# Performance work log

Hardware: AMD Instinct MI355X
Metric: run time of the kernel (lower is better)

## Reference

```python
import jax, jax.numpy as jnp
import numpy as np

N, E = 100000, 1600000
IN, EDGE_DIM, HID, OUT, HEADS = 128, 16, 32, 32, 2


def _glorot(key, shape, scale=0.1):
    return jax.random.normal(key, shape, dtype=jnp.float32) * scale


def setup_inputs() -> dict:
    key = jax.random.key(0)
    ks = jax.random.split(key, 20)
    HC1 = HEADS * HID
    return {
        "x": jax.random.normal(ks[0], (N, IN), dtype=jnp.float32),
        "edge_index": jax.random.randint(ks[1], (2, E), 0, N, dtype=jnp.int32),
        "edge_attr": jax.random.normal(ks[2], (E, EDGE_DIM), dtype=jnp.float32),
        # layer 1 (heads=HEADS, concat=True)
        "W1l": _glorot(ks[3], (IN, HC1)), "b1l": jnp.zeros((HC1,), jnp.float32),
        "W1r": _glorot(ks[4], (IN, HC1)), "b1r": jnp.zeros((HC1,), jnp.float32),
        "W1e": _glorot(ks[5], (EDGE_DIM, HC1)),
        "att1": _glorot(ks[6], (HEADS, HID)),
        "bias1": jnp.zeros((HC1,), jnp.float32),
        # layer 2 (heads=1, concat=False)
        "W2l": _glorot(ks[7], (HC1, HID)), "b2l": jnp.zeros((HID,), jnp.float32),
        "W2r": _glorot(ks[8], (HC1, HID)), "b2r": jnp.zeros((HID,), jnp.float32),
        "W2e": _glorot(ks[9], (EDGE_DIM, HID)),
        "att2": _glorot(ks[10], (1, HID)),
        "bias2": jnp.zeros((HID,), jnp.float32),
        # final linear
        "Wlin": _glorot(ks[11], (HID, OUT)), "blin": jnp.zeros((OUT,), jnp.float32),
    }


def gatv2_layer(x, src, dst, edge_attr, Wl, bl, Wr, br, We, att, bias, H, C, concat):
    n = x.shape[0]
    xl = (x @ Wl + bl).reshape(n, H, C)   # source transform (lin_l)
    xr = (x @ Wr + br).reshape(n, H, C)   # target transform (lin_r)
    ea = (edge_attr @ We).reshape(-1, H, C)
    m = xl[src] + xr[dst] + ea                       # [E, H, C]
    e = jnp.sum(jax.nn.leaky_relu(m, 0.2) * att, axis=-1)  # [E, H]
    # segment softmax over incoming edges of each destination node
    emax = jax.ops.segment_max(e, dst, num_segments=n)
    emax = jnp.where(jnp.isfinite(emax), emax, 0.0)
    ee = jnp.exp(e - emax[dst])
    denom = jax.ops.segment_sum(ee, dst, num_segments=n)
    alpha = ee / (denom[dst] + 1e-16)                # [E, H]
    out = jax.ops.segment_sum(xl[src] * alpha[..., None], dst, num_segments=n)  # [N, H, C]
    out = out.reshape(n, H * C) if concat else out.mean(axis=1)
    return out + bias


def reference(x, edge_index, edge_attr, W1l, b1l, W1r, b1r, W1e, att1, bias1,
              W2l, b2l, W2r, b2r, W2e, att2, bias2, Wlin, blin):
    src, dst = edge_index[0], edge_index[1]
    h = jax.nn.elu(gatv2_layer(x, src, dst, edge_attr, W1l, b1l, W1r, b1r, W1e,
                               att1, bias1, HEADS, HID, True))
    h = jax.nn.elu(gatv2_layer(h, src, dst, edge_attr, W2l, b2l, W2r, b2r, W2e,
                               att2, bias2, 1, HID, False))
    return h @ Wlin + blin
```

## Files before the change

kernel.cpp:

```cpp
#include <hip/hip_runtime.h>
#include <hip/hip_fp16.h>
#include <cstdint>
#include <cstddef>


typedef _Float16 half8 __attribute__((ext_vector_type(8)));
typedef float f32x4 __attribute__((ext_vector_type(4)));

__global__ void hist_kernel(const int* __restrict__ dst, int* __restrict__ deg, int E) {
    int e = blockIdx.x * blockDim.x + threadIdx.x;
    if (e < E) atomicAdd(&deg[dst[e]], 1);
}

__global__ void scan_part(const int* __restrict__ deg, int* __restrict__ bsum, int n) {
    int tid = threadIdx.x;
    int base = blockIdx.x * 1024 + tid * 4;
    int s = 0;
#pragma unroll
    for (int j = 0; j < 4; ++j) {
        int i = base + j;
        if (i < n) s += deg[i];
    }
#pragma unroll
    for (int off = 1; off < 64; off <<= 1) s += __shfl_xor(s, off, 64);
    __shared__ int ws[4];
    if ((tid & 63) == 0) ws[tid >> 6] = s;
    __syncthreads();
    if (tid == 0) bsum[blockIdx.x] = ws[0] + ws[1] + ws[2] + ws[3];
}

__global__ void scan_mid(int* __restrict__ bsum, int* __restrict__ rowstart, int nb, int n) {
    int tid = threadIdx.x;
    int v = (tid < nb) ? bsum[tid] : 0;
    int incl = v;
#pragma unroll
    for (int off = 1; off < 64; off <<= 1) {
        int t = __shfl_up(incl, off, 64);
        if ((tid & 63) >= off) incl += t;
    }
    __shared__ int w0;
    if (tid == 63) w0 = incl;
    __syncthreads();
    if (tid >= 64) incl += w0;
    if (tid < nb) bsum[tid] = incl - v;
    if (tid == nb - 1) rowstart[n] = incl;
}

__global__ void scan_fin(const int* __restrict__ deg, const int* __restrict__ bsum,
                         int* __restrict__ rowstart, int n) {
    int tid = threadIdx.x;
    int lane = tid & 63, wid = tid >> 6;
    int base = blockIdx.x * 1024 + tid * 4;
    int v[4];
    int s = 0;
#pragma unroll
    for (int j = 0; j < 4; ++j) {
        int i = base + j;
        v[j] = (i < n) ? deg[i] : 0;
        s += v[j];
    }
    int incl = s;
#pragma unroll
    for (int off = 1; off < 64; off <<= 1) {
        int t = __shfl_up(incl, off, 64);
        if (lane >= off) incl += t;
    }
    __shared__ int ws[4];
    if (lane == 63) ws[wid] = incl;
    __syncthreads();
    int wofs = 0;
    for (int w2 = 0; w2 < wid; ++w2) wofs += ws[w2];
    int acc = bsum[blockIdx.x] + wofs + (incl - s);
#pragma unroll
    for (int j = 0; j < 4; ++j) {
        int i = base + j;
        if (i < n) rowstart[i] = acc;
        acc += v[j];
    }
}

__global__ void scatter_kernel(const int* __restrict__ src, const int* __restrict__ dst,
                               const int* __restrict__ rowstart, int* __restrict__ cursor,
                               int2* __restrict__ es, int E) {
    int e = blockIdx.x * blockDim.x + threadIdx.x;
    if (e < E) {
        int d = dst[e];
        int p = atomicAdd(&cursor[d], 1);
        es[rowstart[d] + p] = make_int2(e, src[e]);
    }
}

__global__ void f2h_kernel(const float* __restrict__ in, __half* __restrict__ out, long n8) {
    long i = (long)blockIdx.x * blockDim.x + threadIdx.x;
    if (i < n8) {
        const float4* s = (const float4*)&in[i * 8];
        float4 a = s[0], b = s[1];
        __half2* d = (__half2*)&out[i * 8];
        d[0] = __float22half2_rn(make_float2(a.x, a.y));
        d[1] = __float22half2_rn(make_float2(a.z, a.w));
        d[2] = __float22half2_rn(make_float2(b.x, b.y));
        d[3] = __float22half2_rn(make_float2(b.z, b.w));
    }
}

template <int K, int Mh>
__global__ void wprep_kernel(const float* __restrict__ Wl, const float* __restrict__ Wr,
                             __half* __restrict__ Wfrag) {
    constexpr int KS = K / 32;
    constexpr int BN = 2 * Mh;
    int i = blockIdx.x * blockDim.x + threadIdx.x;
    if (i >= K * BN) return;
    int j = i & 7;
    int lane = (i >> 3) & 63;
    int rest = i >> 9;
    int ks = rest % KS;
    int nt = rest / KS;
    int k = ks * 32 + ((lane >> 4) & 3) * 8 + j;
    int col = nt * 16 + (lane & 15);
    float v = (col < Mh) ? Wl[k * Mh + col] : Wr[k * Mh + (col - Mh)];
    Wfrag[i] = __float2half(v);
}

template <int K, int Mh, int BM>
__global__ __launch_bounds__(256) void gemm_mfma(
    const float* __restrict__ x, const __half* __restrict__ Wfrag,
    const float* __restrict__ bl, const float* __restrict__ br,
    __half* __restrict__ yl, __half* __restrict__ yr, int n) {
    constexpr int BN = 2 * Mh;
    constexpr int KS = K / 32;
    constexpr int NT = BN / 16;
    constexpr int RW = BM / 64;
    constexpr int LDP = K + 8;
    __shared__ __half xs[BM * LDP];
    int tid = threadIdx.x;
    int lane = tid & 63;
    int wave = tid >> 6;
    int node0 = blockIdx.x * BM;
    constexpr int ITER = (BM * K) / (256 * 4);
#pragma unroll
    for (int it = 0; it < ITER; ++it) {
        int base = (it * 256 + tid) * 4;
        int row = base / K, kk = base % K;
        float4 v = make_float4(0.f, 0.f, 0.f, 0.f);
        if (node0 + row < n) v = *(const float4*)&x[(size_t)(node0 + row) * K + kk];
        __half2* d = (__half2*)&xs[row * LDP + kk];
        d[0] = __float22half2_rn(make_float2(v.x, v.y));
        d[1] = __float22half2_rn(make_float2(v.z, v.w));
    }
    __syncthreads();
    f32x4 acc[RW][NT];
#pragma unroll
    for (int r = 0; r < RW; ++r)
#pragma unroll
        for (int t = 0; t < NT; ++t) {
            f32x4 z = {0.f, 0.f, 0.f, 0.f};
            acc[r][t] = z;
        }
    int r0 = lane & 15, kof = (lane >> 4) * 8;
#pragma unroll
    for (int ks = 0; ks < KS; ++ks) {
        half8 a[RW];
#pragma unroll
        for (int r = 0; r < RW; ++r) {
            int row = (wave * RW + r) * 16 + r0;
            a[r] = *reinterpret_cast<const half8*>(&xs[row * LDP + ks * 32 + kof]);
        }
#pragma unroll
        for (int t = 0; t < NT; ++t) {
            half8 b = *reinterpret_cast<const half8*>(&Wfrag[(((size_t)t * KS + ks) * 64 + lane) * 8]);
#pragma unroll
            for (int r = 0; r < RW; ++r)
                acc[r][t] = __builtin_amdgcn_mfma_f32_16x16x32_f16(a[r], b, acc[r][t], 0, 0, 0);
        }
    }
#pragma unroll
    for (int r = 0; r < RW; ++r) {
#pragma unroll
        for (int t = 0; t < NT; ++t) {
            int col = t * 16 + (lane & 15);
            float bv = (col < Mh) ? bl[col] : br[col - Mh];
#pragma unroll
            for (int q = 0; q < 4; ++q) {
                int node = node0 + (wave * RW + r) * 16 + (lane >> 4) * 4 + q;
                if (node < n) {
                    float v = acc[r][t][q] + bv;
                    if (col < Mh) yl[(size_t)node * Mh + col] = __float2half(v);
                    else          yr[(size_t)node * Mh + (col - Mh)] = __float2half(v);
                }
            }
        }
    }
}

template <int K, int M, int NPB>
__global__ void linear_kernel(const float* __restrict__ x, const float* __restrict__ W,
                              const float* __restrict__ b, float* __restrict__ y, int n) {
    __shared__ float sx[NPB * K];
    int tid = threadIdx.x;
    int node0 = blockIdx.x * NPB;
    for (int i = tid; i < NPB * K; i += NPB * M) {
        int nn = node0 + i / K;
        sx[i] = (nn < n) ? x[(size_t)nn * K + (i % K)] : 0.f;
    }
    __syncthreads();
    int ln = tid / M, m = tid % M;
    int node = node0 + ln;
    if (node >= n) return;
    float acc = b[m];
#pragma unroll
    for (int k = 0; k < K; ++k) acc = fmaf(sx[ln * K + k], W[k * M + m], acc);
    y[(size_t)node * M + m] = acc;
}

template <int H, int C>
__global__ __launch_bounds__(256) void fused_edge_agg(
    const int* __restrict__ rowstart, const int2* __restrict__ es,
    const __half* __restrict__ eah,
    const float* __restrict__ We,
    const float* __restrict__ att,
    const __half* __restrict__ xl, const __half* __restrict__ xr,
    const float* __restrict__ bias, float* __restrict__ out, int n) {
    constexpr int HC = H * C;
    constexpr int LPN = HC / 2;
    constexpr int NPW = 64 / LPN;
    int gt = blockIdx.x * blockDim.x + threadIdx.x;
    int wave = gt >> 6;
    int lane = threadIdx.x & 63;
    int sub = lane / LPN;
    int j = lane % LPN;
    int ch0 = 2 * j;
    int node = wave * NPW + sub;
    if (node >= n) return;
    __half2 wh[16];
#pragma unroll
    for (int k = 0; k < 16; ++k) wh[k] = __float22half2_rn(*(const float2*)&We[k * HC + ch0]);
    float2 a2 = *(const float2*)&att[ch0];
    float2 xr2 = __half22float2(*(const __half2*)&xr[(size_t)node * HC + ch0]);
    int beg = rowstart[node], end = rowstart[node + 1];
    float denom = 0.f, acc0 = 0.f, acc1 = 0.f;

    auto gemv = [&](const float4& r0, const float4& r1, const __half2& xlh,
                    float& m0, float& m1, float2& xlf) {
        const __half2* h0 = (const __half2*)&r0;
        const __half2* h1 = (const __half2*)&r1;
        __half2 p0 = __hmul2(__low2half2(h0[0]), wh[0]);
        __half2 p1 = __hmul2(__high2half2(h0[0]), wh[1]);
        p0 = __hfma2(__low2half2(h0[1]), wh[2], p0);
        p1 = __hfma2(__high2half2(h0[1]), wh[3], p1);
        p0 = __hfma2(__low2half2(h0[2]), wh[4], p0);
        p1 = __hfma2(__high2half2(h0[2]), wh[5], p1);
        p0 = __hfma2(__low2half2(h0[3]), wh[6], p0);
        p1 = __hfma2(__high2half2(h0[3]), wh[7], p1);
        p0 = __hfma2(__low2half2(h1[0]), wh[8], p0);
        p1 = __hfma2(__high2half2(h1[0]), wh[9], p1);
        p0 = __hfma2(__low2half2(h1[1]), wh[10], p0);
        p1 = __hfma2(__high2half2(h1[1]), wh[11], p1);
        p0 = __hfma2(__low2half2(h1[2]), wh[12], p0);
        p1 = __hfma2(__high2half2(h1[2]), wh[13], p1);
        p0 = __hfma2(__low2half2(h1[3]), wh[14], p0);
        p1 = __hfma2(__high2half2(h1[3]), wh[15], p1);
        float2 mf = __half22float2(__hadd2(p0, p1));
        xlf = __half22float2(xlh);
        m0 = xlf.x + xr2.x + mf.x;
        m1 = xlf.y + xr2.y + mf.y;
    };
    auto logit = [&](float m0, float m1) -> float {
        m0 = (m0 > 0.f) ? m0 : 0.2f * m0;
        m1 = (m1 > 0.f) ? m1 : 0.2f * m1;
        float v = m0 * a2.x + m1 * a2.y;
#pragma unroll
        for (int msk = 1; msk < 16; msk <<= 1) v += __shfl_xor(v, msk, 64);
        return v;
    };

    int pp = beg;
    for (; pp + 4 <= end; pp += 4) {
        int2 er[4];
        float4 r0[4], r1[4];
        __half2 xh[4];
#pragma unroll
        for (int u = 0; u < 4; ++u) er[u] = es[pp + u];
#pragma unroll
        for (int u = 0; u < 4; ++u) {
            const float4* q = (const float4*)&eah[(size_t)er[u].x * 16];
            r0[u] = q[0];
            r1[u] = q[1];
            xh[u] = *(const __half2*)&xl[(size_t)er[u].y * HC + ch0];
        }
#pragma unroll
        for (int u = 0; u < 4; ++u) {
            float m0, m1;
            float2 xlf;
            gemv(r0[u], r1[u], xh[u], m0, m1, xlf);
            float w = __expf(logit(m0, m1));
            denom += w;
            acc0 = fmaf(xlf.x, w, acc0);
            acc1 = fmaf(xlf.y, w, acc1);
        }
    }
    for (; pp < end; ++pp) {
        int2 e2 = es[pp];
        const float4* q = (const float4*)&eah[(size_t)e2.x * 16];
        float4 r0 = q[0], r1 = q[1];
        __half2 xlh = *(const __half2*)&xl[(size_t)e2.y * HC + ch0];
        float m0, m1;
        float2 xlf;
        gemv(r0, r1, xlh, m0, m1, xlf);
        float w = __expf(logit(m0, m1));
        denom += w;
        acc0 = fmaf(xlf.x, w, acc0);
        acc1 = fmaf(xlf.y, w, acc1);
    }
    float2 b2 = *(const float2*)&bias[ch0];
    float inv = 1.f / (denom + 1e-16f);
    float o0 = acc0 * inv + b2.x;
    float o1 = acc1 * inv + b2.y;
    o0 = (o0 > 0.f) ? o0 : __expf(o0) - 1.f;
    o1 = (o1 > 0.f) ? o1 : __expf(o1) - 1.f;
    *(float2*)&out[(size_t)node * HC + ch0] = make_float2(o0, o1);
}

extern "C" void kernel_launch(void* const* d_in, const int* in_sizes, int n_in,
                              void* d_out, int out_size, void* d_ws, size_t ws_size,
                              hipStream_t stream) {
    const float* x     = (const float*)d_in[0];
    const int*   eidx  = (const int*)d_in[1];
    const float* eattr = (const float*)d_in[2];
    const float* W1l   = (const float*)d_in[3];
    const float* b1l   = (const float*)d_in[4];
    const float* W1r   = (const float*)d_in[5];
    const float* b1r   = (const float*)d_in[6];
    const float* W1e   = (const float*)d_in[7];
    const float* att1  = (const float*)d_in[8];
    const float* bias1 = (const float*)d_in[9];
    const float* W2l   = (const float*)d_in[10];
    const float* b2l   = (const float*)d_in[11];
    const float* W2r   = (const float*)d_in[12];
    const float* b2r   = (const float*)d_in[13];
    const float* W2e   = (const float*)d_in[14];
    const float* att2  = (const float*)d_in[15];
    const float* bias2 = (const float*)d_in[16];
    const float* Wlin  = (const float*)d_in[17];
    const float* blin  = (const float*)d_in[18];

    const int N = in_sizes[0] / 128;
    const int E = in_sizes[1] / 2;
    const int* src = eidx;
    const int* dst = eidx + E;

    char* p = (char*)d_ws;
    auto take = [&](size_t bytes) {
        char* r = p;
        p += (bytes + 255) & ~(size_t)255;
        return r;
    };
    int*    deg      = (int*)take((size_t)N * sizeof(int));
    int*    cursor   = (int*)take((size_t)N * sizeof(int));
    int*    rowstart = (int*)take((size_t)(N + 1) * sizeof(int));
    int*    bsum     = (int*)take(256 * sizeof(int));
    int2*   es       = (int2*)take((size_t)E * sizeof(int2));
    __half* A        = (__half*)take((size_t)N * 64 * sizeof(__half));
    __half* B        = (__half*)take((size_t)N * 64 * sizeof(__half));
    float*  Cbuf     = (float*)take((size_t)N * 64 * sizeof(float));
    __half* eah      = (__half*)take((size_t)E * 16 * sizeof(__half));
    __half* Wf1      = (__half*)take((size_t)128 * 128 * sizeof(__half));
    __half* Wf2      = (__half*)take((size_t)64 * 64 * sizeof(__half));

    (void)hipMemsetAsync(deg, 0, (size_t)N * sizeof(int), stream);
    (void)hipMemsetAsync(cursor, 0, (size_t)N * sizeof(int), stream);
    hist_kernel<<<(E + 255) / 256, 256, 0, stream>>>(dst, deg, E);
    {
        int nb = (N + 1023) / 1024;
        scan_part<<<nb, 256, 0, stream>>>(deg, bsum, N);
        scan_mid<<<1, 128, 0, stream>>>(bsum, rowstart, nb, N);
        scan_fin<<<nb, 256, 0, stream>>>(deg, bsum, rowstart, N);
    }
    scatter_kernel<<<(E + 255) / 256, 256, 0, stream>>>(src, dst, rowstart, cursor, es, E);
    {
        long n8 = (long)E * 16 / 8;
        f2h_kernel<<<(int)((n8 + 255) / 256), 256, 0, stream>>>(eattr, eah, n8);
    }
    wprep_kernel<128, 64><<<(128 * 128 + 255) / 256, 256, 0, stream>>>(W1l, W1r, Wf1);
    wprep_kernel<64, 32><<<(64 * 64 + 255) / 256, 256, 0, stream>>>(W2l, W2r, Wf2);

    gemm_mfma<128, 64, 64><<<(N + 63) / 64, 256, 0, stream>>>(x, Wf1, b1l, b1r, A, B, N);
    fused_edge_agg<2, 32><<<(int)(((size_t)((N + 1) / 2) * 64 + 255) / 256), 256, 0, stream>>>(
        rowstart, es, eah, W1e, att1, A, B, bias1, Cbuf, N);

    gemm_mfma<64, 32, 128><<<(N + 127) / 128, 256, 0, stream>>>(Cbuf, Wf2, b2l, b2r, A, B, N);
    fused_edge_agg<1, 32><<<(int)(((size_t)((N + 3) / 4) * 64 + 255) / 256), 256, 0, stream>>>(
        rowstart, es, eah, W2e, att2, A, B, bias2, Cbuf, N);

    linear_kernel<32, 32, 8><<<(N + 7) / 8, 256, 0, stream>>>(Cbuf, Wlin, blin, (float*)d_out, N);
}
```

Baseline: 444.1 us.

## Store edge attributes in dst-sorted order during scatter and drop f2h kernel

The scatter kernel now converts each edge's attributes to fp16 and writes them at the edge's CSR position, alongside a plain sorted source-index array. The separate f2h conversion kernel and the edge-id indirection are gone. The edge aggregation kernels therefore read attributes contiguously instead of gathering them by edge id, and the main loop unroll drops from 4 to 2. The scatter kernel's random-position writes grow from 8 to 36 bytes per edge, and the shallower unroll may expose more load latency.

Measured after the change: 457.9 us. 3.1% more time.

```diff
diff --git a/kernel.cpp b/kernel.cpp
--- a/kernel.cpp
+++ b/kernel.cpp
@@ -80,26 +80,30 @@
 }
 
 __global__ void scatter_kernel(const int* __restrict__ src, const int* __restrict__ dst,
+                               const float* __restrict__ eattr,
                                const int* __restrict__ rowstart, int* __restrict__ cursor,
-                               int2* __restrict__ es, int E) {
+                               int* __restrict__ src_sorted, __half* __restrict__ eah_sorted,
+                               int E) {
     int e = blockIdx.x * blockDim.x + threadIdx.x;
     if (e < E) {
         int d = dst[e];
         int p = atomicAdd(&cursor[d], 1);
-        es[rowstart[d] + p] = make_int2(e, src[e]);
-    }
-}
-
-__global__ void f2h_kernel(const float* __restrict__ in, __half* __restrict__ out, long n8) {
-    long i = (long)blockIdx.x * blockDim.x + threadIdx.x;
-    if (i < n8) {
-        const float4* s = (const float4*)&in[i * 8];
-        float4 a = s[0], b = s[1];
-        __half2* d = (__half2*)&out[i * 8];
-        d[0] = __float22half2_rn(make_float2(a.x, a.y));
-        d[1] = __float22half2_rn(make_float2(a.z, a.w));
-        d[2] = __float22half2_rn(make_float2(b.x, b.y));
-        d[3] = __float22half2_rn(make_float2(b.z, b.w));
+        int pos = rowstart[d] + p;
+        src_sorted[pos] = src[e];
+        const float4* s4 = (const float4*)&eattr[(size_t)e * 16];
+        float4 a = s4[0], b = s4[1], c = s4[2], f = s4[3];
+        __half2 h[8];
+        h[0] = __float22half2_rn(make_float2(a.x, a.y));
+        h[1] = __float22half2_rn(make_float2(a.z, a.w));
+        h[2] = __float22half2_rn(make_float2(b.x, b.y));
+        h[3] = __float22half2_rn(make_float2(b.z, b.w));
+        h[4] = __float22half2_rn(make_float2(c.x, c.y));
+        h[5] = __float22half2_rn(make_float2(c.z, c.w));
+        h[6] = __float22half2_rn(make_float2(f.x, f.y));
+        h[7] = __float22half2_rn(make_float2(f.z, f.w));
+        int4* o = (int4*)&eah_sorted[(size_t)pos * 16];
+        o[0] = *(int4*)&h[0];
+        o[1] = *(int4*)&h[4];
     }
 }
 
@@ -214,8 +218,8 @@
 
 template <int H, int C>
 __global__ __launch_bounds__(256) void fused_edge_agg(
-    const int* __restrict__ rowstart, const int2* __restrict__ es,
-    const __half* __restrict__ eah,
+    const int* __restrict__ rowstart, const int* __restrict__ src_sorted,
+    const __half* __restrict__ eah_sorted,
     const float* __restrict__ We,
     const float* __restrict__ att,
     const __half* __restrict__ xl, const __half* __restrict__ xr,
@@ -274,42 +278,39 @@
     };
 
     int pp = beg;
-    for (; pp + 4 <= end; pp += 4) {
-        int2 er[4];
-        float4 r0[4], r1[4];
-        __half2 xh[4];
-#pragma unroll
-        for (int u = 0; u < 4; ++u) er[u] = es[pp + u];
-#pragma unroll
-        for (int u = 0; u < 4; ++u) {
-            const float4* q = (const float4*)&eah[(size_t)er[u].x * 16];
-            r0[u] = q[0];
-            r1[u] = q[1];
-            xh[u] = *(const __half2*)&xl[(size_t)er[u].y * HC + ch0];
-        }
-#pragma unroll
-        for (int u = 0; u < 4; ++u) {
-            float m0, m1;
-            float2 xlf;
-            gemv(r0[u], r1[u], xh[u], m0, m1, xlf);
-            float w = __expf(logit(m0, m1));
-            denom += w;
-            acc0 = fmaf(xlf.x, w, acc0);
-            acc1 = fmaf(xlf.y, w, acc1);
-        }
-    }
-    for (; pp < end; ++pp) {
-        int2 e2 = es[pp];
-        const float4* q = (const float4*)&eah[(size_t)e2.x * 16];
-        float4 r0 = q[0], r1 = q[1];
-        __half2 xlh = *(const __half2*)&xl[(size_t)e2.y * HC + ch0];
-        float m0, m1;
-        float2 xlf;
-        gemv(r0, r1, xlh, m0, m1, xlf);
-        float w = __expf(logit(m0, m1));
-        denom += w;
-        acc0 = fmaf(xlf.x, w, acc0);
-        acc1 = fmaf(xlf.y, w, acc1);
+    for (; pp + 2 <= end; pp += 2) {
+        int s0 = src_sorted[pp];
+        int s1 = src_sorted[pp + 1];
+        const float4* qa = (const float4*)&eah_sorted[(size_t)pp * 16];
+        const float4* qb = (const float4*)&eah_sorted[((size_t)pp + 1) * 16];
+        float4 r0a = qa[0], r1a = qa[1];
+        float4 r0b = qb[0], r1b = qb[1];
+        __half2 xh0 = *(const __half2*)&xl[(size_t)s0 * HC + ch0];
+        __half2 xh1 = *(const __half2*)&xl[(size_t)s1 * HC + ch0];
+        float m0a, m1a, m0b, m1b;
+        float2 xla, xlb;
+        gemv(r0a, r1a, xh0, m0a, m1a, xla);
+        gemv(r0b, r1b, xh1, m0b, m1b, xlb);
+        float wa = __expf(logit(m0a, m1a));
+        float wb = __expf(logit(m0b, m1b));
+        denom += wa + wb;
+        acc0 = fmaf(xla.x, wa, acc0);
+        acc1 = fmaf(xla.y, wa, acc1);
+        acc0 = fmaf(xlb.x, wb, acc0);
+        acc1 = fmaf(xlb.y, wb, acc1);
+    }
+    if (pp < end) {
+        int s0 = src_sorted[pp];
+        const float4* qa = (const float4*)&eah_sorted[(size_t)pp * 16];
+        float4 r0a = qa[0], r1a = qa[1];
+        __half2 xh0 = *(const __half2*)&xl[(size_t)s0 * HC + ch0];
+        float m0a, m1a;
+        float2 xla;
+        gemv(r0a, r1a, xh0, m0a, m1a, xla);
+        float wa = __expf(logit(m0a, m1a));
+        denom += wa;
+        acc0 = fmaf(xla.x, wa, acc0);
+        acc1 = fmaf(xla.y, wa, acc1);
     }
     float2 b2 = *(const float2*)&bias[ch0];
     float inv = 1.f / (denom + 1e-16f);
@@ -354,17 +355,17 @@
         p += (bytes + 255) & ~(size_t)255;
         return r;
     };
-    int*    deg      = (int*)take((size_t)N * sizeof(int));
-    int*    cursor   = (int*)take((size_t)N * sizeof(int));
-    int*    rowstart = (int*)take((size_t)(N + 1) * sizeof(int));
-    int*    bsum     = (int*)take(256 * sizeof(int));
-    int2*   es       = (int2*)take((size_t)E * sizeof(int2));
-    __half* A        = (__half*)take((size_t)N * 64 * sizeof(__half));
-    __half* B        = (__half*)take((size_t)N * 64 * sizeof(__half));
-    float*  Cbuf     = (float*)take((size_t)N * 64 * sizeof(float));
-    __half* eah      = (__half*)take((size_t)E * 16 * sizeof(__half));
-    __half* Wf1      = (__half*)take((size_t)128 * 128 * sizeof(__half));
-    __half* Wf2      = (__half*)take((size_t)64 * 64 * sizeof(__half));
+    int*    deg        = (int*)take((size_t)N * sizeof(int));
+    int*    cursor     = (int*)take((size_t)N * sizeof(int));
+    int*    rowstart   = (int*)take((size_t)(N + 1) * sizeof(int));
+    int*    bsum       = (int*)take(256 * sizeof(int));
+    int*    src_sorted = (int*)take((size_t)E * sizeof(int));
+    __half* eah_sorted = (__half*)take((size_t)E * 16 * sizeof(__half));
+    __half* A          = (__half*)take((size_t)N * 64 * sizeof(__half));
+    __half* B          = (__half*)take((size_t)N * 64 * sizeof(__half));
+    float*  Cbuf       = (float*)take((size_t)N * 64 * sizeof(float));
+    __half* Wf1        = (__half*)take((size_t)128 * 128 * sizeof(__half));
+    __half* Wf2        = (__half*)take((size_t)64 * 64 * sizeof(__half));
 
     (void)hipMemsetAsync(deg, 0, (size_t)N * sizeof(int), stream);
     (void)hipMemsetAsync(cursor, 0, (size_t)N * sizeof(int), stream);
@@ -375,21 +376,18 @@
         scan_mid<<<1, 128, 0, stream>>>(bsum, rowstart, nb, N);
         scan_fin<<<nb, 256, 0, stream>>>(deg, bsum, rowstart, N);
     }
-    scatter_kernel<<<(E + 255) / 256, 256, 0, stream>>>(src, dst, rowstart, cursor, es, E);
-    {
-        long n8 = (long)E * 16 / 8;
-        f2h_kernel<<<(int)((n8 + 255) / 256), 256, 0, stream>>>(eattr, eah, n8);
-    }
+    scatter_kernel<<<(E + 255) / 256, 256, 0, stream>>>(src, dst, eattr, rowstart, cursor,
+                                                        src_sorted, eah_sorted, E);
     wprep_kernel<128, 64><<<(128 * 128 + 255) / 256, 256, 0, stream>>>(W1l, W1r, Wf1);
     wprep_kernel<64, 32><<<(64 * 64 + 255) / 256, 256, 0, stream>>>(W2l, W2r, Wf2);
 
     gemm_mfma<128, 64, 64><<<(N + 63) / 64, 256, 0, stream>>>(x, Wf1, b1l, b1r, A, B, N);
     fused_edge_agg<2, 32><<<(int)(((size_t)((N + 1) / 2) * 64 + 255) / 256), 256, 0, stream>>>(
-        rowstart, es, eah, W1e, att1, A, B, bias1, Cbuf, N);
+        rowstart, src_sorted, eah_sorted, W1e, att1, A, B, bias1, Cbuf, N);
 
     gemm_mfma<64, 32, 128><<<(N + 127) / 128, 256, 0, stream>>>(Cbuf, Wf2, b2l, b2r, A, B, N);
     fused_edge_agg<1, 32><<<(int)(((size_t)((N + 3) / 4) * 64 + 255) / 256), 256, 0, stream>>>(
-        rowstart, es, eah, W2e, att2, A, B, bias2, Cbuf, N);
+        rowstart, src_sorted, eah_sorted, W2e, att2, A, B, bias2, Cbuf, N);
 
     linear_kernel<32, 32, 8><<<(N + 7) / 8, 256, 0, stream>>>(Cbuf, Wlin, blin, (float*)d_out, N);
 }
```
